# Kernel optimization log

Measured on AMD Instinct MI355X. Metric: run time of the kernel, lower is better.

The kernel has to match this reference:

```python
import jax, jax.numpy as jnp
import numpy as np

H = 12     # attention heads
W1S = 256  # one-sided sliding window (attention_window = 512)
NW = 8     # n_windows -> global tokens at each window start


def ln(x, g, b, eps=1e-5):
    m = jnp.mean(x, -1, keepdims=True)
    v = jnp.mean(jnp.square(x - m), -1, keepdims=True)
    return (x - m) * jax.lax.rsqrt(v + eps) * g + b


def _forward(x, x_mask, word_emb, pos_emb, emb_g, emb_b, Wq, bq, Wk, bk, Wv, bv, Wo, bo,
             Wqg, bqg, Wkg, bkg, Wvg, bvg, ln1_g, ln1_b, W1, b1, W2, b2, ln2_g, ln2_b,
             out_w, out_b):
    B, S = x.shape
    D = word_emb.shape[1]
    Dh = D // H
    w = W1S
    nb = S // w
    win_len = S // NW
    g = NW
    gpos = jnp.arange(g) * win_len
    scale = 1.0 / np.sqrt(Dh)

    x_mask = x_mask.at[:, gpos].set(1)  # module forces global slots to be valid
    kmask = x_mask > 0
    is_glob = jnp.zeros((S,), bool).at[gpos].set(True)

    h = ln(word_emb[x] + pos_emb[None], emb_g, emb_b)

    # static masks for the banded (sliding-window) scores
    kidx = jnp.arange(nb)[:, None] * w + jnp.arange(3 * w)[None, :] - w  # [nb,3w] abs key idx
    in_rng = (kidx >= 0) & (kidx < S)
    kidx_c = jnp.clip(kidx, 0, S - 1)
    key_ok = in_rng[None] & kmask[:, kidx_c] & (~is_glob[kidx_c])[None]   # [B,nb,3w]
    diff = jnp.arange(3 * w)[None, :] - w - jnp.arange(w)[:, None]        # [w,3w] key-query offset
    band_mask = ((jnp.abs(diff) <= w)[None, None] & key_ok[:, :, None, :]).reshape(B, 1, S, 3 * w)
    gkey_mask = kmask[:, gpos][:, None, None, :]                           # [B,1,1,g]
    mask_all = jnp.concatenate([jnp.broadcast_to(gkey_mask, (B, 1, S, g)),
                                jnp.broadcast_to(band_mask, (B, 1, S, 3 * w))], -1)

    def heads(t):
        return t.reshape(B, S, H, Dh).transpose(0, 2, 1, 3)

    def chunk3(t):  # [B,H,S,Dh] -> [B,H,nb,3w,Dh]; block n covers key offsets [-w, 2w)
        tp = jnp.pad(t, ((0, 0), (0, 0), (w, w), (0, 0))).reshape(B, H, nb + 2, w, Dh)
        return jnp.concatenate([tp[:, :, :nb], tp[:, :, 1:nb + 1], tp[:, :, 2:]], axis=3)

    def layer(h, p):
        (wq, bq_, wk, bk_, wv, bv_, wo, bo_, wqg, bqg_, wkg, bkg_, wvg, bvg_,
         g1, gb1, w1, fb1, w2, fb2, g2, gb2) = p
        q = heads(h @ wq + bq_); k = heads(h @ wk + bk_); v = heads(h @ wv + bv_)
        # sliding-window band scores + extra global-key columns, joint softmax
        sb = jnp.einsum('bhnqd,bhnkd->bhnqk', q.reshape(B, H, nb, w, Dh), chunk3(k)) * scale
        sg = jnp.einsum('bhsd,bhgd->bhsg', q, k[:, :, gpos]) * scale
        scores = jnp.concatenate([sg, sb.reshape(B, H, S, 3 * w)], -1)
        neg = jnp.finfo(scores.dtype).min * 0.5
        probs = jax.nn.softmax(jnp.where(mask_all, scores, neg), -1)
        ctx = (jnp.einsum('bhnqk,bhnkd->bhnqd', probs[..., g:].reshape(B, H, nb, w, 3 * w), chunk3(v)).reshape(B, H, S, Dh)
               + jnp.einsum('bhsg,bhgd->bhsd', probs[..., :g], v[:, :, gpos]))
        ctx = ctx.transpose(0, 2, 1, 3).reshape(B, S, D)
        # global-token queries: full attention over all keys with separate projections
        qg = (h[:, gpos] @ wqg + bqg_).reshape(B, g, H, Dh).transpose(0, 2, 1, 3)
        kg = heads(h @ wkg + bkg_); vg = heads(h @ wvg + bvg_)
        sgl = jnp.where(kmask[:, None, None, :], jnp.einsum('bhgd,bhsd->bhgs', qg, kg) * scale, neg)
        ctxg = jnp.einsum('bhgs,bhsd->bhgd', jax.nn.softmax(sgl, -1), vg).transpose(0, 2, 1, 3).reshape(B, g, D)
        ctx = ctx.at[:, gpos].set(ctxg)
        h = ln(h + ctx @ wo + bo_, g1, gb1)
        h = ln(h + jax.nn.gelu(h @ w1 + fb1, approximate=False) @ w2 + fb2, g2, gb2)
        return h, None

    params = (Wq, bq, Wk, bk, Wv, bv, Wo, bo, Wqg, bqg, Wkg, bkg, Wvg, bvg,
              ln1_g, ln1_b, W1, b1, W2, b2, ln2_g, ln2_b)
    h, _ = jax.lax.scan(jax.checkpoint(layer), h, params)
    y = h.reshape(B * NW, win_len, D)[:, 0]   # CLS pooling per window
    return y @ out_w + out_b


def setup_inputs():
    key = jax.random.key(0)
    V, S, D, L, F, O, B = 50265, 4096, 768, 12, 3072, 128, 1
    ks = iter(jax.random.split(key, 40))
    def nrm(shape):
        return (jax.random.normal(next(ks), shape) * 0.02).astype(jnp.float32)
    inp = {
        'x': jax.random.randint(next(ks), (B, S), 0, V, dtype=jnp.int32),
        'x_mask': jnp.ones((B, S), jnp.int32),
        'word_emb': nrm((V, D)), 'pos_emb': nrm((S, D)),
        'emb_g': jnp.ones((D,)), 'emb_b': jnp.zeros((D,)),
        'Wq': nrm((L, D, D)), 'bq': jnp.zeros((L, D)),
        'Wk': nrm((L, D, D)), 'bk': jnp.zeros((L, D)),
        'Wv': nrm((L, D, D)), 'bv': jnp.zeros((L, D)),
        'Wo': nrm((L, D, D)), 'bo': jnp.zeros((L, D)),
        'Wqg': nrm((L, D, D)), 'bqg': jnp.zeros((L, D)),
        'Wkg': nrm((L, D, D)), 'bkg': jnp.zeros((L, D)),
        'Wvg': nrm((L, D, D)), 'bvg': jnp.zeros((L, D)),
        'ln1_g': jnp.ones((L, D)), 'ln1_b': jnp.zeros((L, D)),
        'W1': nrm((L, D, F)), 'b1': jnp.zeros((L, F)),
        'W2': nrm((L, F, D)), 'b2': jnp.zeros((L, D)),
        'ln2_g': jnp.ones((L, D)), 'ln2_b': jnp.zeros((L, D)),
        'out_w': nrm((D, O)), 'out_b': jnp.zeros((O,)),
    }
    return inp


def reference(x, x_mask, word_emb, pos_emb, emb_g, emb_b, Wq, bq, Wk, bk, Wv, bv, Wo, bo,
              Wqg, bqg, Wkg, bkg, Wvg, bvg, ln1_g, ln1_b, W1, b1, W2, b2, ln2_g, ln2_b,
              out_w, out_b):
    return _forward(x, x_mask, word_emb, pos_emb, emb_g, emb_b, Wq, bq, Wk, bk, Wv, bv,
                    Wo, bo, Wqg, bqg, Wkg, bkg, Wvg, bvg, ln1_g, ln1_b, W1, b1, W2, b2,
                    ln2_g, ln2_b, out_w, out_b)
```

## Files before the change

### kernel.cpp

```cpp
#include <hip/hip_runtime.h>
#include <cstddef>

#define S_LEN   4096
#define DMODEL  768
#define NHEAD   12
#define DHEAD   64
#define FDIM    3072
#define NLAYER  12
#define WIN     256
#define NGLOB   8
#define GSTRIDE 512

typedef short bf16x8 __attribute__((ext_vector_type(8)));
typedef float f32x4 __attribute__((ext_vector_type(4)));
typedef unsigned short u16;

__device__ __forceinline__ u16 f2bf(float f) {
  unsigned u = __builtin_bit_cast(unsigned, f);
  return (u16)((u + 0x7FFFu + ((u >> 16) & 1u)) >> 16);
}
__device__ __forceinline__ float bf2f(u16 s) {
  unsigned u = ((unsigned)s) << 16;
  return __builtin_bit_cast(float, u);
}

__device__ __forceinline__ void gload16(const void* g, void* l) {
  __builtin_amdgcn_global_load_lds(
      (const __attribute__((address_space(1))) void*)g,
      (__attribute__((address_space(3))) void*)l, 16, 0, 0);
}

__device__ __forceinline__ float wave_sum(float v) {
#pragma unroll
  for (int off = 32; off > 0; off >>= 1) v += __shfl_xor(v, off);
  return v;
}

__device__ __forceinline__ float block_sum256(float v, float* sbuf) {
  v = wave_sum(v);
  int w = threadIdx.x >> 6;
  __syncthreads();
  if ((threadIdx.x & 63) == 0) sbuf[w] = v;
  __syncthreads();
  return sbuf[0] + sbuf[1] + sbuf[2] + sbuf[3];
}

__global__ __launch_bounds__(256) void embed_ln_kernel(
    const int* __restrict__ x, const float* __restrict__ wemb,
    const float* __restrict__ pemb, const float* __restrict__ gg,
    const float* __restrict__ bb, float* __restrict__ h, u16* __restrict__ hb) {
  __shared__ float sbuf[4];
  int s = blockIdx.x, tid = threadIdx.x;
  int idx = x[s];
  float vals[3];
#pragma unroll
  for (int i = 0; i < 3; i++) {
    int d = tid + i * 256;
    vals[i] = wemb[(size_t)idx * DMODEL + d] + pemb[(size_t)s * DMODEL + d];
  }
  float mean = block_sum256(vals[0] + vals[1] + vals[2], sbuf) * (1.0f / 768.0f);
  float sq = 0.f;
#pragma unroll
  for (int i = 0; i < 3; i++) { float t = vals[i] - mean; sq += t * t; }
  float inv = rsqrtf(block_sum256(sq, sbuf) * (1.0f / 768.0f) + 1e-5f);
#pragma unroll
  for (int i = 0; i < 3; i++) {
    int d = tid + i * 256;
    float r = (vals[i] - mean) * inv * gg[d] + bb[d];
    h[(size_t)s * DMODEL + d] = r;
    hb[(size_t)s * DMODEL + d] = f2bf(r);
  }
}

__global__ __launch_bounds__(256) void add_ln_kernel(
    float* __restrict__ h, const float* __restrict__ r,
    const float* __restrict__ gg, const float* __restrict__ bb,
    u16* __restrict__ hb) {
  __shared__ float sbuf[4];
  int s = blockIdx.x, tid = threadIdx.x;
  float vals[3];
#pragma unroll
  for (int i = 0; i < 3; i++) {
    int d = tid + i * 256;
    vals[i] = h[(size_t)s * DMODEL + d] + r[(size_t)s * DMODEL + d];
  }
  float mean = block_sum256(vals[0] + vals[1] + vals[2], sbuf) * (1.0f / 768.0f);
  float sq = 0.f;
#pragma unroll
  for (int i = 0; i < 3; i++) { float t = vals[i] - mean; sq += t * t; }
  float inv = rsqrtf(block_sum256(sq, sbuf) * (1.0f / 768.0f) + 1e-5f);
#pragma unroll
  for (int i = 0; i < 3; i++) {
    int d = tid + i * 256;
    float rr = (vals[i] - mean) * inv * gg[d] + bb[d];
    h[(size_t)s * DMODEL + d] = rr;
    hb[(size_t)s * DMODEL + d] = f2bf(rr);
  }
}

#define DD_ ((size_t)DMODEL * DMODEL)
#define DF_ ((size_t)DMODEL * FDIM)
#define WSTRIDE (6 * DD_ + 2 * DF_)
__global__ __launch_bounds__(256) void convw_kernel(
    const float* __restrict__ Wq, const float* __restrict__ Wk,
    const float* __restrict__ Wv, const float* __restrict__ Wkg,
    const float* __restrict__ Wvg, const float* __restrict__ Wo,
    const float* __restrict__ W1, const float* __restrict__ W2,
    u16* __restrict__ wt) {
  int l = blockIdx.y;
  int bid = blockIdx.x;
  const float* src; u16* dst; int K, N, r;
  u16* base = wt + (size_t)l * WSTRIDE;
  if (bid < 864) {
    int m = bid / 144; r = bid % 144; K = 768; N = 768;
    switch (m) {
      case 0: src = Wq  + l * DD_; dst = base;           break;
      case 1: src = Wk  + l * DD_; dst = base + 1 * DD_; break;
      case 2: src = Wv  + l * DD_; dst = base + 2 * DD_; break;
      case 3: src = Wkg + l * DD_; dst = base + 3 * DD_; break;
      case 4: src = Wvg + l * DD_; dst = base + 4 * DD_; break;
      default: src = Wo + l * DD_; dst = base + 5 * DD_; break;
    }
  } else if (bid < 1440) {
    r = bid - 864; K = 768; N = 3072; src = W1 + l * DF_; dst = base + 6 * DD_;
  } else {
    r = bid - 1440; K = 3072; N = 768; src = W2 + l * DF_; dst = base + 6 * DD_ + DF_;
  }
  int nt = N / 64;
  int tk = (r / nt) * 64, tn = (r % nt) * 64;
  int t = threadIdx.x;
  int c = t >> 2, ko = t & 3;
#pragma unroll
  for (int p = 0; p < 2; p++) {
    int kb = (p * 4 + ko) * 8;
    const float* sp = src + (size_t)(tk + kb) * N + tn + c;
    bf16x8 val;
#pragma unroll
    for (int j = 0; j < 8; j++) val[j] = (short)f2bf(sp[(size_t)j * N]);
    *(bf16x8*)&dst[(size_t)(tn + c) * K + tk + kb] = val;
  }
}

template <int ACT, int OUTM, int TM>
__device__ __forceinline__ void mm_core(const u16* __restrict__ A, const u16* __restrict__ Wt,
                                        const float* __restrict__ bias, void* __restrict__ Cv,
                                        int M, int N, int K, int bm, int bn,
                                        u16* As, u16* Bs) {
  constexpr int MR = TM / 32;
  constexpr int AJ = TM / 32;
  int t = threadIdx.x;
  int wid = t >> 6, lane = t & 63;
  int wr = (wid >> 1) * (TM / 2), wc = (wid & 1) * 64;
  int lr = lane & 15, lg = lane >> 4;
  f32x4 acc[MR][4];
  f32x4 zf = {0.f, 0.f, 0.f, 0.f};
#pragma unroll
  for (int m = 0; m < MR; m++)
#pragma unroll
    for (int n = 0; n < 4; n++) acc[m][n] = zf;

  int srow = wid * 8 + (lane >> 3);
  int sgr = (lane & 7) ^ (lane >> 3);
  const u16* aSrc = A + (size_t)(bm + srow) * K + sgr * 8;
  const u16* bSrc = Wt + (size_t)(bn + srow) * K + sgr * 8;
  int dstOff = wid * 8 * 64;

  for (int kt = 0; kt < K; kt += 64) {
    __syncthreads();
#pragma unroll
    for (int j = 0; j < AJ; j++)
      gload16(aSrc + kt + (size_t)j * 32 * K, As + dstOff + j * 32 * 64);
#pragma unroll
    for (int j = 0; j < 4; j++)
      gload16(bSrc + kt + (size_t)j * 32 * K, Bs + dstOff + j * 32 * 64);
    __syncthreads();
#pragma unroll
    for (int ks = 0; ks < 2; ks++) {
      bf16x8 af[MR], bfr[4];
#pragma unroll
      for (int m = 0; m < MR; m++)
        af[m] = *(const bf16x8*)&As[(wr + m * 16 + lr) * 64 + (((ks * 4 + lg) ^ (lr & 7)) * 8)];
#pragma unroll
      for (int n = 0; n < 4; n++)
        bfr[n] = *(const bf16x8*)&Bs[(wc + n * 16 + lr) * 64 + (((ks * 4 + lg) ^ (lr & 7)) * 8)];
#pragma unroll
      for (int m = 0; m < MR; m++)
#pragma unroll
        for (int n = 0; n < 4; n++)
          acc[m][n] = __builtin_amdgcn_mfma_f32_16x16x32_bf16(af[m], bfr[n], acc[m][n], 0, 0, 0);
    }
  }
#pragma unroll
  for (int n = 0; n < 4; n++) {
    int col = bn + wc + n * 16 + lr;
    float bb = bias[col];
#pragma unroll
    for (int m = 0; m < MR; m++) {
#pragma unroll
      for (int r = 0; r < 4; r++) {
        int row = bm + wr + m * 16 + lg * 4 + r;
        float xv = acc[m][n][r] + bb;
        if (ACT == 1) xv = 0.5f * xv * (1.0f + erff(xv * 0.70710678118654752f));
        if (OUTM == 0) ((float*)Cv)[(size_t)row * N + col] = xv;
        else if (OUTM == 1) ((u16*)Cv)[(size_t)row * N + col] = f2bf(xv);
        else ((u16*)Cv)[(size_t)col * M + row] = f2bf(xv);
      }
    }
  }
}

template <int ACT, int OUTM, int TM>
__global__ __launch_bounds__(256) void mm_kernel(const u16* A, const u16* Wt, const float* bias,
                                                 void* Cv, int M, int N, int K) {
  __shared__ u16 As[TM * 64];
  __shared__ u16 Bs[128 * 64];
  mm_core<ACT, OUTM, TM>(A, Wt, bias, Cv, M, N, K, blockIdx.y * TM, blockIdx.x * 128, As, Bs);
}

__global__ __launch_bounds__(256) void mm5_kernel(
    const u16* A,
    const u16* W0, const u16* W1_, const u16* W2_, const u16* W3, const u16* W4,
    const float* b0, const float* b1, const float* b2, const float* b3, const float* b4,
    u16* C0, u16* C1, u16* C2, u16* C3, u16* C4, int M, int K,
    const float* __restrict__ h, const float* __restrict__ Wqg,
    const float* __restrict__ bqg, float* __restrict__ qg) {
  __shared__ u16 As[128 * 64];
  __shared__ u16 Bs[128 * 64];
  if (blockIdx.x == 30) {
    int b = blockIdx.y;
    if (b >= 24) return;
    int gi = b / 3, c0 = (b % 3) * 256;
    int tid = threadIdx.x;
    float* hs = (float*)As;
    const float* hrow = h + (size_t)gi * GSTRIDE * DMODEL;
    for (int i = tid; i < DMODEL; i += 256) hs[i] = hrow[i];
    __syncthreads();
    float a = bqg[c0 + tid];
    for (int k = 0; k < DMODEL; k++) a += hs[k] * Wqg[(size_t)k * DMODEL + c0 + tid];
    qg[gi * DMODEL + c0 + tid] = a;
    return;
  }
  int which = blockIdx.x / 6;
  int bn = (blockIdx.x % 6) * 128;
  const u16* Ws[5] = {W0, W1_, W2_, W3, W4};
  const float* bs[5] = {b0, b1, b2, b3, b4};
  u16* Cs[5] = {C0, C1, C2, C3, C4};
  if (which == 2 || which == 4)
    mm_core<0, 2, 128>(A, Ws[which], bs[which], Cs[which], M, DMODEL, K, blockIdx.y * 128, bn, As, Bs);
  else
    mm_core<0, 1, 128>(A, Ws[which], bs[which], Cs[which], M, DMODEL, K, blockIdx.y * 128, bn, As, Bs);
}

__device__ __forceinline__ void sliding_body(
    int bid, u16* Ps,
    const u16* __restrict__ qb, const u16* __restrict__ kb,
    const u16* __restrict__ vt, const int* __restrict__ xmask,
    u16* __restrict__ ctx) {
  int hh = bid >> 5;
  int q0 = (bid & 31) * 128;
  int w = threadIdx.x >> 6, lane = threadIdx.x & 63;
  int lr = lane & 15, lg = lane >> 4;
  int rowb = q0 + w * 32;
  f32x4 zf = {0.f, 0.f, 0.f, 0.f};
  u16* Pw = Ps + w * 2048;

  bf16x8 qf[2][2];
#pragma unroll
  for (int mf = 0; mf < 2; mf++) {
    const u16* qptr = qb + (size_t)(rowb + mf * 16 + lr) * DMODEL + hh * DHEAD;
    qf[mf][0] = *(const bf16x8*)(qptr + lg * 8);
    qf[mf][1] = *(const bf16x8*)(qptr + 32 + lg * 8);
  }

  float m_run[2][4], l_run[2][4];
  f32x4 ctxa[2][4];
#pragma unroll
  for (int mf = 0; mf < 2; mf++)
#pragma unroll
    for (int r = 0; r < 4; r++) {
      m_run[mf][r] = -1e30f; l_run[mf][r] = 0.f; ctxa[mf][r] = zf;
    }

  {
    int krow = (lr < NGLOB) ? lr * GSTRIDE : 0;
    const u16* kp = kb + (size_t)krow * DMODEL + hh * DHEAD + lg * 8;
    bf16x8 kf0 = *(const bf16x8*)kp;
    bf16x8 kf1 = *(const bf16x8*)(kp + 32);
#pragma unroll
    for (int mf = 0; mf < 2; mf++) {
      f32x4 sa = __builtin_amdgcn_mfma_f32_16x16x32_bf16(qf[mf][0], kf0, zf, 0, 0, 0);
      sa = __builtin_amdgcn_mfma_f32_16x16x32_bf16(qf[mf][1], kf1, sa, 0, 0, 0);
      float p0[4], tmax[4];
#pragma unroll
      for (int r = 0; r < 4; r++) {
        float s = (lr < NGLOB) ? sa[r] * 0.125f : -1e30f;
        p0[r] = s; tmax[r] = s;
      }
#pragma unroll
      for (int o = 8; o; o >>= 1)
#pragma unroll
        for (int r = 0; r < 4; r++) tmax[r] = fmaxf(tmax[r], __shfl_xor(tmax[r], o));
      float tsum[4];
#pragma unroll
      for (int r = 0; r < 4; r++) {
        m_run[mf][r] = tmax[r];
        p0[r] = __expf(p0[r] - tmax[r]);
        tsum[r] = p0[r];
      }
#pragma unroll
      for (int o = 8; o; o >>= 1)
#pragma unroll
        for (int r = 0; r < 4; r++) tsum[r] += __shfl_xor(tsum[r], o);
#pragma unroll
      for (int r = 0; r < 4; r++) l_run[mf][r] = tsum[r];
#pragma unroll
      for (int r = 0; r < 4; r++) {
        int qi = mf * 16 + lg * 4 + r;
        Pw[qi * 64 + (((lr >> 3) ^ (qi & 7)) * 8) + (lr & 7)] = f2bf(p0[r]);
        int k2 = 16 + lr;
        Pw[qi * 64 + (((k2 >> 3) ^ (qi & 7)) * 8) + (k2 & 7)] = 0;
      }
    }
    bf16x8 pf0 = *(const bf16x8*)&Pw[lr * 64 + ((lg ^ (lr & 7)) * 8)];
    bf16x8 pf1 = *(const bf16x8*)&Pw[(16 + lr) * 64 + ((lg ^ (lr & 7)) * 8)];
#pragma unroll
    for (int c2 = 0; c2 < 4; c2++) {
      bf16x8 vg8 = {0, 0, 0, 0, 0, 0, 0, 0};
      if (lg == 0) {
        const u16* vrow = vt + (size_t)(hh * DHEAD + c2 * 16 + lr) * S_LEN;
#pragma unroll
        for (int j = 0; j < 8; j++) vg8[j] = (short)vrow[(size_t)j * GSTRIDE];
      }
      ctxa[0][c2] = __builtin_amdgcn_mfma_f32_16x16x32_bf16(pf0, vg8, ctxa[0][c2], 0, 0, 0);
      ctxa[1][c2] = __builtin_amdgcn_mfma_f32_16x16x32_bf16(pf1, vg8, ctxa[1][c2], 0, 0, 0);
    }
  }

  for (int tt = 0; tt < 10; tt++) {
    int base = q0 - WIN + tt * 64;
    if (base + 63 < 0 || base >= S_LEN) continue;
    bf16x8 kf[4][2];
    int keyc[4]; bool vc[4];
#pragma unroll
    for (int c = 0; c < 4; c++) {
      int key = base + c * 16 + lr;
      int krow = key < 0 ? 0 : (key > S_LEN - 1 ? S_LEN - 1 : key);
      vc[c] = (key >= 0) && (key < S_LEN) && ((key & (GSTRIDE - 1)) != 0) && (xmask[krow] != 0);
      keyc[c] = key;
      const u16* kp = kb + (size_t)krow * DMODEL + hh * DHEAD + lg * 8;
      kf[c][0] = *(const bf16x8*)kp;
      kf[c][1] = *(const bf16x8*)(kp + 32);
    }
#pragma unroll
    for (int mf = 0; mf < 2; mf++) {
      f32x4 sa[4];
#pragma unroll
      for (int c = 0; c < 4; c++) {
        sa[c] = __builtin_amdgcn_mfma_f32_16x16x32_bf16(qf[mf][0], kf[c][0], zf, 0, 0, 0);
        sa[c] = __builtin_amdgcn_mfma_f32_16x16x32_bf16(qf[mf][1], kf[c][1], sa[c], 0, 0, 0);
      }
      float p[4][4], tmax[4] = {-1e30f, -1e30f, -1e30f, -1e30f};
#pragma unroll
      for (int c = 0; c < 4; c++)
#pragma unroll
        for (int r = 0; r < 4; r++) {
          int qrow = rowb + mf * 16 + lg * 4 + r;
          int dd = keyc[c] - qrow;
          float s = (vc[c] && dd >= -WIN && dd <= WIN) ? sa[c][r] * 0.125f : -1e30f;
          p[c][r] = s;
          tmax[r] = fmaxf(tmax[r], s);
        }
#pragma unroll
      for (int o = 8; o; o >>= 1)
#pragma unroll
        for (int r = 0; r < 4; r++) tmax[r] = fmaxf(tmax[r], __shfl_xor(tmax[r], o));
      float sc[4], tsum[4] = {0.f, 0.f, 0.f, 0.f};
#pragma unroll
      for (int r = 0; r < 4; r++) {
        float mn = fmaxf(m_run[mf][r], tmax[r]);
        sc[r] = __expf(m_run[mf][r] - mn);
        m_run[mf][r] = mn;
      }
#pragma unroll
      for (int c = 0; c < 4; c++)
#pragma unroll
        for (int r = 0; r < 4; r++) {
          p[c][r] = __expf(p[c][r] - m_run[mf][r]);
          tsum[r] += p[c][r];
        }
#pragma unroll
      for (int o = 8; o; o >>= 1)
#pragma unroll
        for (int r = 0; r < 4; r++) tsum[r] += __shfl_xor(tsum[r], o);
#pragma unroll
      for (int r = 0; r < 4; r++) l_run[mf][r] = l_run[mf][r] * sc[r] + tsum[r];
#pragma unroll
      for (int c2 = 0; c2 < 4; c2++)
#pragma unroll
        for (int r = 0; r < 4; r++) ctxa[mf][c2][r] *= sc[r];
#pragma unroll
      for (int c = 0; c < 4; c++)
#pragma unroll
        for (int r = 0; r < 4; r++) {
          int qi = mf * 16 + lg * 4 + r, k64 = c * 16 + lr;
          Pw[qi * 64 + (((k64 >> 3) ^ (qi & 7)) * 8) + (k64 & 7)] = f2bf(p[c][r]);
        }
    }
#pragma unroll
    for (int ks = 0; ks < 2; ks++) {
      bf16x8 pf0 = *(const bf16x8*)&Pw[lr * 64 + (((ks * 4 + lg) ^ (lr & 7)) * 8)];
      bf16x8 pf1 = *(const bf16x8*)&Pw[(16 + lr) * 64 + (((ks * 4 + lg) ^ (lr & 7)) * 8)];
      int kstart = base + ks * 32 + lg * 8;
      int kc = kstart < 0 ? 0 : (kstart > S_LEN - 8 ? S_LEN - 8 : kstart);
#pragma unroll
      for (int c2 = 0; c2 < 4; c2++) {
        const u16* vp = vt + (size_t)(hh * DHEAD + c2 * 16 + lr) * S_LEN + kc;
        bf16x8 vf = *(const bf16x8*)vp;
        ctxa[0][c2] = __builtin_amdgcn_mfma_f32_16x16x32_bf16(pf0, vf, ctxa[0][c2], 0, 0, 0);
        ctxa[1][c2] = __builtin_amdgcn_mfma_f32_16x16x32_bf16(pf1, vf, ctxa[1][c2], 0, 0, 0);
      }
    }
  }

#pragma unroll
  for (int mf = 0; mf < 2; mf++)
#pragma unroll
    for (int c2 = 0; c2 < 4; c2++)
#pragma unroll
      for (int r = 0; r < 4; r++) {
        int qrow = rowb + mf * 16 + lg * 4 + r;
        ctx[(size_t)qrow * DMODEL + hh * DHEAD + c2 * 16 + lr] = f2bf(ctxa[mf][c2][r] / l_run[mf][r]);
      }
}

__device__ __forceinline__ void gattn_body(
    int hh, int c, u16* Ps,
    const float* __restrict__ qg, const u16* __restrict__ kg,
    const u16* __restrict__ vgt, const int* __restrict__ xmask,
    float* __restrict__ pm, float* __restrict__ pl, float* __restrict__ pacc) {
  int w = threadIdx.x >> 6, lane = threadIdx.x & 63;
  int lr = lane & 15, lg = lane >> 4;
  int base = c * 256 + w * 64;
  f32x4 zf = {0.f, 0.f, 0.f, 0.f};

  bf16x8 qf0, qf1;
  {
    const float* qp = qg + (size_t)(lr & 7) * DMODEL + hh * DHEAD;
    bool real = lr < 8;
#pragma unroll
    for (int j = 0; j < 8; j++) {
      qf0[j] = real ? (short)f2bf(0.125f * qp[lg * 8 + j]) : (short)0;
      qf1[j] = real ? (short)f2bf(0.125f * qp[32 + lg * 8 + j]) : (short)0;
    }
  }

  f32x4 sa[4];
  bool vc[4];
#pragma unroll
  for (int st = 0; st < 4; st++) {
    int key = base + st * 16 + lr;
    vc[st] = (xmask[key] != 0) || ((key & (GSTRIDE - 1)) == 0);
    const u16* kp = kg + (size_t)key * DMODEL + hh * DHEAD + lg * 8;
    sa[st] = __builtin_amdgcn_mfma_f32_16x16x32_bf16(qf0, *(const bf16x8*)kp, zf, 0, 0, 0);
    sa[st] = __builtin_amdgcn_mfma_f32_16x16x32_bf16(qf1, *(const bf16x8*)(kp + 32), sa[st], 0, 0, 0);
  }
  float p[4][4], tmax[4] = {-1e30f, -1e30f, -1e30f, -1e30f};
#pragma unroll
  for (int st = 0; st < 4; st++)
#pragma unroll
    for (int r = 0; r < 4; r++) {
      float s = vc[st] ? sa[st][r] : -1e30f;
      p[st][r] = s;
      tmax[r] = fmaxf(tmax[r], s);
    }
#pragma unroll
  for (int o = 8; o; o >>= 1)
#pragma unroll
    for (int r = 0; r < 4; r++) tmax[r] = fmaxf(tmax[r], __shfl_xor(tmax[r], o));
  float tsum[4] = {0.f, 0.f, 0.f, 0.f};
#pragma unroll
  for (int st = 0; st < 4; st++)
#pragma unroll
    for (int r = 0; r < 4; r++) {
      float pv = vc[st] ? __expf(p[st][r] - tmax[r]) : 0.f;
      p[st][r] = pv;
      tsum[r] += pv;
    }
#pragma unroll
  for (int o = 8; o; o >>= 1)
#pragma unroll
    for (int r = 0; r < 4; r++) tsum[r] += __shfl_xor(tsum[r], o);
#pragma unroll
  for (int st = 0; st < 4; st++)
#pragma unroll
    for (int r = 0; r < 4; r++) {
      int qi = lg * 4 + r, k64 = st * 16 + lr;
      Ps[w * 1024 + qi * 64 + (((k64 >> 3) ^ (qi & 7)) * 8) + (k64 & 7)] = f2bf(p[st][r]);
    }
  f32x4 ctxa[4] = {zf, zf, zf, zf};
#pragma unroll
  for (int ks = 0; ks < 2; ks++) {
    bf16x8 pf = *(const bf16x8*)&Ps[w * 1024 + lr * 64 + (((ks * 4 + lg) ^ (lr & 7)) * 8)];
    int kstart = base + ks * 32 + lg * 8;
#pragma unroll
    for (int c2 = 0; c2 < 4; c2++) {
      const u16* vp = vgt + (size_t)(hh * DHEAD + c2 * 16 + lr) * S_LEN + kstart;
      ctxa[c2] = __builtin_amdgcn_mfma_f32_16x16x32_bf16(pf, *(const bf16x8*)vp, ctxa[c2], 0, 0, 0);
    }
  }
  int pidx = (hh * 16 + c) * 4 + w;
  if (lg < 2) {
#pragma unroll
    for (int r = 0; r < 4; r++) {
      int q = lg * 4 + r;
#pragma unroll
      for (int c2 = 0; c2 < 4; c2++)
        pacc[(size_t)pidx * 512 + q * 64 + c2 * 16 + lr] = ctxa[c2][r];
      if (lr == 0) {
        pm[pidx * 8 + q] = tmax[r];
        pl[pidx * 8 + q] = tsum[r];
      }
    }
  }
}

__global__ __launch_bounds__(256) void attn_kernel(
    const u16* __restrict__ qb, const u16* __restrict__ kb,
    const u16* __restrict__ vt, const int* __restrict__ xmask,
    u16* __restrict__ ctx,
    const float* __restrict__ qg, const u16* __restrict__ kg,
    const u16* __restrict__ vgt,
    float* __restrict__ pm, float* __restrict__ pl, float* __restrict__ pacc) {
  __shared__ u16 Ps[4 * 32 * 64];
  int bid = blockIdx.x;
  if (bid < NHEAD * 32) {
    sliding_body(bid, Ps, qb, kb, vt, xmask, ctx);
  } else {
    int idx = bid - NHEAD * 32;
    gattn_body(idx >> 4, idx & 15, Ps, qg, kg, vgt, xmask, pm, pl, pacc);
  }
}

__global__ __launch_bounds__(64) void gattn_comb_kernel(
    const float* __restrict__ pm, const float* __restrict__ pl,
    const float* __restrict__ pacc, u16* __restrict__ ctx) {
  int gi = blockIdx.x / NHEAD, hh = blockIdx.x % NHEAD;
  int d = threadIdx.x;
  float M = -1e30f, L = 0.f, A = 0.f;
  for (int i = 0; i < 64; i++) {
    int pidx = hh * 64 + i;
    float m_i = pm[pidx * 8 + gi];
    float l_i = pl[pidx * 8 + gi];
    float a_i = pacc[(size_t)pidx * 512 + gi * 64 + d];
    if (m_i > M) {
      float sc = __expf(M - m_i);
      A = A * sc + a_i;
      L = L * sc + l_i;
      M = m_i;
    } else {
      float sc = __expf(m_i - M);
      A += a_i * sc;
      L += l_i * sc;
    }
  }
  ctx[(size_t)gi * GSTRIDE * DMODEL + hh * DHEAD + d] = f2bf(A / L);
}

__global__ __launch_bounds__(128) void cls_out_kernel(
    const float* __restrict__ h, const float* __restrict__ ow,
    const float* __restrict__ ob, float* __restrict__ y) {
  __shared__ float hs[DMODEL];
  int wi = blockIdx.x;
  int tid = threadIdx.x;
  for (int i = tid; i < DMODEL; i += 128) hs[i] = h[(size_t)wi * GSTRIDE * DMODEL + i];
  __syncthreads();
  float a = ob[tid];
  for (int d = 0; d < DMODEL; d++) a += hs[d] * ow[d * 128 + tid];
  y[wi * 128 + tid] = a;
}

extern "C" void kernel_launch(void* const* d_in, const int* in_sizes, int n_in,
                              void* d_out, int out_size, void* d_ws, size_t ws_size,
                              hipStream_t stream) {
  const int*   x      = (const int*)d_in[0];
  const int*   xmask  = (const int*)d_in[1];
  const float* wemb   = (const float*)d_in[2];
  const float* pemb   = (const float*)d_in[3];
  const float* emb_g  = (const float*)d_in[4];
  const float* emb_b  = (const float*)d_in[5];
  const float* Wq     = (const float*)d_in[6];
  const float* bq     = (const float*)d_in[7];
  const float* Wk     = (const float*)d_in[8];
  const float* bk     = (const float*)d_in[9];
  const float* Wv     = (const float*)d_in[10];
  const float* bv     = (const float*)d_in[11];
  const float* Wo     = (const float*)d_in[12];
  const float* bo     = (const float*)d_in[13];
  const float* Wqg    = (const float*)d_in[14];
  const float* bqg    = (const float*)d_in[15];
  const float* Wkg    = (const float*)d_in[16];
  const float* bkg    = (const float*)d_in[17];
  const float* Wvg    = (const float*)d_in[18];
  const float* bvg    = (const float*)d_in[19];
  const float* ln1_g  = (const float*)d_in[20];
  const float* ln1_b  = (const float*)d_in[21];
  const float* W1     = (const float*)d_in[22];
  const float* b1     = (const float*)d_in[23];
  const float* W2     = (const float*)d_in[24];
  const float* b2     = (const float*)d_in[25];
  const float* ln2_g  = (const float*)d_in[26];
  const float* ln2_b  = (const float*)d_in[27];
  const float* out_w  = (const float*)d_in[28];
  const float* out_b  = (const float*)d_in[29];

  char* wsp = (char*)d_ws;
  float* h   = (float*)wsp;  wsp += (size_t)S_LEN * DMODEL * 4;
  float* tmp = (float*)wsp;  wsp += (size_t)S_LEN * DMODEL * 4;
  u16* hb  = (u16*)wsp;      wsp += (size_t)S_LEN * DMODEL * 2;
  u16* ctx = (u16*)wsp;      wsp += (size_t)S_LEN * DMODEL * 2;
  u16* qb  = (u16*)wsp;      wsp += (size_t)S_LEN * DMODEL * 2;
  u16* kb  = (u16*)wsp;      wsp += (size_t)S_LEN * DMODEL * 2;
  u16* vt  = (u16*)wsp;      wsp += (size_t)S_LEN * DMODEL * 2;
  u16* kgb = (u16*)wsp;      wsp += (size_t)S_LEN * DMODEL * 2;
  u16* vgt = (u16*)wsp;      wsp += (size_t)S_LEN * DMODEL * 2;
  u16* mid = (u16*)wsp;      wsp += (size_t)S_LEN * FDIM * 2;
  float* qgb = (float*)wsp;  wsp += (size_t)NGLOB * DMODEL * 4;
  float* pm = (float*)wsp;   wsp += (size_t)768 * 8 * 4;
  float* pl = (float*)wsp;   wsp += (size_t)768 * 8 * 4;
  float* pacc = (float*)wsp; wsp += (size_t)768 * 512 * 4;
  u16* wtb = (u16*)wsp;      wsp += WSTRIDE * NLAYER * 2;

  embed_ln_kernel<<<S_LEN, 256, 0, stream>>>(x, wemb, pemb, emb_g, emb_b, h, hb);
  convw_kernel<<<dim3(2016, NLAYER), 256, 0, stream>>>(Wq, Wk, Wv, Wkg, Wvg, Wo, W1, W2, wtb);

  for (int l = 0; l < NLAYER; l++) {
    const float* bql  = bq  + (size_t)l * DMODEL;
    const float* bkl  = bk  + (size_t)l * DMODEL;
    const float* bvl  = bv  + (size_t)l * DMODEL;
    const float* bol  = bo  + (size_t)l * DMODEL;
    const float* wqg  = Wqg + (size_t)l * DD_;
    const float* bqgl = bqg + (size_t)l * DMODEL;
    const float* bkgl = bkg + (size_t)l * DMODEL;
    const float* bvgl = bvg + (size_t)l * DMODEL;
    const float* b1l  = b1  + (size_t)l * FDIM;
    const float* b2l  = b2  + (size_t)l * DMODEL;
    u16* base = wtb + (size_t)l * WSTRIDE;
    u16* wqT  = base;
    u16* wkT  = base + 1 * DD_;
    u16* wvT  = base + 2 * DD_;
    u16* wkgT = base + 3 * DD_;
    u16* wvgT = base + 4 * DD_;
    u16* woT  = base + 5 * DD_;
    u16* w1T  = base + 6 * DD_;
    u16* w2T  = base + 6 * DD_ + DF_;

    mm5_kernel<<<dim3(31, 32), 256, 0, stream>>>(
        hb, wqT, wkT, wvT, wkgT, wvgT, bql, bkl, bvl, bkgl, bvgl,
        qb, kb, vt, kgb, vgt, S_LEN, DMODEL, h, wqg, bqgl, qgb);

    attn_kernel<<<NHEAD * 32 + NHEAD * 16, 256, 0, stream>>>(
        qb, kb, vt, xmask, ctx, qgb, kgb, vgt, pm, pl, pacc);
    gattn_comb_kernel<<<NGLOB * NHEAD, 64, 0, stream>>>(pm, pl, pacc, ctx);

    mm_kernel<0, 0, 64><<<dim3(6, 64), 256, 0, stream>>>(ctx, woT, bol, tmp, S_LEN, DMODEL, DMODEL);
    add_ln_kernel<<<S_LEN, 256, 0, stream>>>(h, tmp, ln1_g + (size_t)l * DMODEL,
                                             ln1_b + (size_t)l * DMODEL, hb);

    mm_kernel<1, 1, 128><<<dim3(24, 32), 256, 0, stream>>>(hb, w1T, b1l, mid, S_LEN, FDIM, DMODEL);
    mm_kernel<0, 0, 64><<<dim3(6, 64), 256, 0, stream>>>(mid, w2T, b2l, tmp, S_LEN, DMODEL, FDIM);
    add_ln_kernel<<<S_LEN, 256, 0, stream>>>(h, tmp, ln2_g + (size_t)l * DMODEL,
                                             ln2_b + (size_t)l * DMODEL, hb);
  }

  cls_out_kernel<<<NGLOB, 128, 0, stream>>>(h, out_w, out_b, (float*)d_out);
}
```

Measured before the change: 3.130 ms.

## Fuse global attention combine, swizzle GEMM block order, store residual in bf16

Global-token attention now runs one block per head. Each block loops over all keys with an online softmax and combines its four waves' partial results in shared memory, which removes the separate combine kernel and the global partial buffers. The sliding-window attention no longer writes the global-token rows, and those blocks are scheduled after the global ones. The matmul kernels remap block indices with a stride-8 swizzle to improve cache reuse. The output-projection and FFN2 results are stored in bf16 instead of fp32, halving that traffic at some precision cost. The global-attention path now uses only 12 long serial blocks, which risks leaving the tail of the kernel poorly parallelised.

After: 2.945 ms. 5.9% less time.

```diff
diff --git a/kernel.cpp b/kernel.cpp
--- a/kernel.cpp
+++ b/kernel.cpp
@@ -73,7 +73,7 @@
 }
 
 __global__ __launch_bounds__(256) void add_ln_kernel(
-    float* __restrict__ h, const float* __restrict__ r,
+    float* __restrict__ h, const u16* __restrict__ r,
     const float* __restrict__ gg, const float* __restrict__ bb,
     u16* __restrict__ hb) {
   __shared__ float sbuf[4];
@@ -82,7 +82,7 @@
 #pragma unroll
   for (int i = 0; i < 3; i++) {
     int d = tid + i * 256;
-    vals[i] = h[(size_t)s * DMODEL + d] + r[(size_t)s * DMODEL + d];
+    vals[i] = h[(size_t)s * DMODEL + d] + bf2f(r[(size_t)s * DMODEL + d]);
   }
   float mean = block_sum256(vals[0] + vals[1] + vals[2], sbuf) * (1.0f / 768.0f);
   float sq = 0.f;
@@ -214,7 +214,11 @@
                                                  void* Cv, int M, int N, int K) {
   __shared__ u16 As[TM * 64];
   __shared__ u16 Bs[128 * 64];
-  mm_core<ACT, OUTM, TM>(A, Wt, bias, Cv, M, N, K, blockIdx.y * TM, blockIdx.x * 128, As, Bs);
+  int nwg = gridDim.x * gridDim.y;
+  int lin = blockIdx.y * gridDim.x + blockIdx.x;
+  int swz = (lin & 7) * (nwg >> 3) + (lin >> 3);
+  int bx = swz / gridDim.y, by = swz % gridDim.y;
+  mm_core<ACT, OUTM, TM>(A, Wt, bias, Cv, M, N, K, by * TM, bx * 128, As, Bs);
 }
 
 __global__ __launch_bounds__(256) void mm5_kernel(
@@ -240,15 +244,18 @@
     qg[gi * DMODEL + c0 + tid] = a;
     return;
   }
-  int which = blockIdx.x / 6;
-  int bn = (blockIdx.x % 6) * 128;
+  int lin = blockIdx.y * 30 + blockIdx.x;
+  int swz = (lin & 7) * 120 + (lin >> 3);
+  int bx = swz >> 5, by = swz & 31;
+  int which = bx / 6;
+  int bn = (bx % 6) * 128;
   const u16* Ws[5] = {W0, W1_, W2_, W3, W4};
   const float* bs[5] = {b0, b1, b2, b3, b4};
   u16* Cs[5] = {C0, C1, C2, C3, C4};
   if (which == 2 || which == 4)
-    mm_core<0, 2, 128>(A, Ws[which], bs[which], Cs[which], M, DMODEL, K, blockIdx.y * 128, bn, As, Bs);
+    mm_core<0, 2, 128>(A, Ws[which], bs[which], Cs[which], M, DMODEL, K, by * 128, bn, As, Bs);
   else
-    mm_core<0, 1, 128>(A, Ws[which], bs[which], Cs[which], M, DMODEL, K, blockIdx.y * 128, bn, As, Bs);
+    mm_core<0, 1, 128>(A, Ws[which], bs[which], Cs[which], M, DMODEL, K, by * 128, bn, As, Bs);
 }
 
 __device__ __forceinline__ void sliding_body(
@@ -429,19 +436,20 @@
 #pragma unroll
       for (int r = 0; r < 4; r++) {
         int qrow = rowb + mf * 16 + lg * 4 + r;
-        ctx[(size_t)qrow * DMODEL + hh * DHEAD + c2 * 16 + lr] = f2bf(ctxa[mf][c2][r] / l_run[mf][r]);
+        if ((qrow & (GSTRIDE - 1)) != 0)
+          ctx[(size_t)qrow * DMODEL + hh * DHEAD + c2 * 16 + lr] = f2bf(ctxa[mf][c2][r] / l_run[mf][r]);
       }
 }
 
 __device__ __forceinline__ void gattn_body(
-    int hh, int c, u16* Ps,
+    int hh, u16* Ps, float* cM, float* cL, float* cA,
     const float* __restrict__ qg, const u16* __restrict__ kg,
     const u16* __restrict__ vgt, const int* __restrict__ xmask,
-    float* __restrict__ pm, float* __restrict__ pl, float* __restrict__ pacc) {
+    u16* __restrict__ ctx) {
   int w = threadIdx.x >> 6, lane = threadIdx.x & 63;
   int lr = lane & 15, lg = lane >> 4;
-  int base = c * 256 + w * 64;
   f32x4 zf = {0.f, 0.f, 0.f, 0.f};
+  u16* Pw = Ps + w * 1024;
 
   bf16x8 qf0, qf1;
   {
@@ -454,73 +462,107 @@
     }
   }
 
-  f32x4 sa[4];
-  bool vc[4];
-#pragma unroll
-  for (int st = 0; st < 4; st++) {
-    int key = base + st * 16 + lr;
-    vc[st] = (xmask[key] != 0) || ((key & (GSTRIDE - 1)) == 0);
-    const u16* kp = kg + (size_t)key * DMODEL + hh * DHEAD + lg * 8;
-    sa[st] = __builtin_amdgcn_mfma_f32_16x16x32_bf16(qf0, *(const bf16x8*)kp, zf, 0, 0, 0);
-    sa[st] = __builtin_amdgcn_mfma_f32_16x16x32_bf16(qf1, *(const bf16x8*)(kp + 32), sa[st], 0, 0, 0);
-  }
-  float p[4][4], tmax[4] = {-1e30f, -1e30f, -1e30f, -1e30f};
-#pragma unroll
-  for (int st = 0; st < 4; st++)
+  float m_run[4] = {-1e30f, -1e30f, -1e30f, -1e30f};
+  float l_run[4] = {0.f, 0.f, 0.f, 0.f};
+  f32x4 ctxa[4] = {zf, zf, zf, zf};
+
+  for (int tt = w; tt < 64; tt += 4) {
+    int base = tt * 64;
+    f32x4 sa[4];
+    bool vc[4];
+#pragma unroll
+    for (int st = 0; st < 4; st++) {
+      int key = base + st * 16 + lr;
+      vc[st] = (xmask[key] != 0) || ((key & (GSTRIDE - 1)) == 0);
+      const u16* kp = kg + (size_t)key * DMODEL + hh * DHEAD + lg * 8;
+      sa[st] = __builtin_amdgcn_mfma_f32_16x16x32_bf16(qf0, *(const bf16x8*)kp, zf, 0, 0, 0);
+      sa[st] = __builtin_amdgcn_mfma_f32_16x16x32_bf16(qf1, *(const bf16x8*)(kp + 32), sa[st], 0, 0, 0);
+    }
+    float p[4][4], tmax[4] = {-1e30f, -1e30f, -1e30f, -1e30f};
+#pragma unroll
+    for (int st = 0; st < 4; st++)
+#pragma unroll
+      for (int r = 0; r < 4; r++) {
+        float s = vc[st] ? sa[st][r] : -1e30f;
+        p[st][r] = s;
+        tmax[r] = fmaxf(tmax[r], s);
+      }
+#pragma unroll
+    for (int o = 8; o; o >>= 1)
+#pragma unroll
+      for (int r = 0; r < 4; r++) tmax[r] = fmaxf(tmax[r], __shfl_xor(tmax[r], o));
+    float sc[4], tsum[4] = {0.f, 0.f, 0.f, 0.f};
 #pragma unroll
     for (int r = 0; r < 4; r++) {
-      float s = vc[st] ? sa[st][r] : -1e30f;
-      p[st][r] = s;
-      tmax[r] = fmaxf(tmax[r], s);
-    }
-#pragma unroll
-  for (int o = 8; o; o >>= 1)
-#pragma unroll
-    for (int r = 0; r < 4; r++) tmax[r] = fmaxf(tmax[r], __shfl_xor(tmax[r], o));
-  float tsum[4] = {0.f, 0.f, 0.f, 0.f};
-#pragma unroll
-  for (int st = 0; st < 4; st++)
-#pragma unroll
-    for (int r = 0; r < 4; r++) {
-      float pv = vc[st] ? __expf(p[st][r] - tmax[r]) : 0.f;
-      p[st][r] = pv;
-      tsum[r] += pv;
-    }
-#pragma unroll
-  for (int o = 8; o; o >>= 1)
-#pragma unroll
-    for (int r = 0; r < 4; r++) tsum[r] += __shfl_xor(tsum[r], o);
-#pragma unroll
-  for (int st = 0; st < 4; st++)
-#pragma unroll
-    for (int r = 0; r < 4; r++) {
-      int qi = lg * 4 + r, k64 = st * 16 + lr;
-      Ps[w * 1024 + qi * 64 + (((k64 >> 3) ^ (qi & 7)) * 8) + (k64 & 7)] = f2bf(p[st][r]);
-    }
-  f32x4 ctxa[4] = {zf, zf, zf, zf};
-#pragma unroll
-  for (int ks = 0; ks < 2; ks++) {
-    bf16x8 pf = *(const bf16x8*)&Ps[w * 1024 + lr * 64 + (((ks * 4 + lg) ^ (lr & 7)) * 8)];
-    int kstart = base + ks * 32 + lg * 8;
-#pragma unroll
-    for (int c2 = 0; c2 < 4; c2++) {
-      const u16* vp = vgt + (size_t)(hh * DHEAD + c2 * 16 + lr) * S_LEN + kstart;
-      ctxa[c2] = __builtin_amdgcn_mfma_f32_16x16x32_bf16(pf, *(const bf16x8*)vp, ctxa[c2], 0, 0, 0);
-    }
-  }
-  int pidx = (hh * 16 + c) * 4 + w;
+      float mn = fmaxf(m_run[r], tmax[r]);
+      sc[r] = __expf(m_run[r] - mn);
+      m_run[r] = mn;
+    }
+#pragma unroll
+    for (int st = 0; st < 4; st++)
+#pragma unroll
+      for (int r = 0; r < 4; r++) {
+        float pv = vc[st] ? __expf(p[st][r] - m_run[r]) : 0.f;
+        p[st][r] = pv;
+        tsum[r] += pv;
+      }
+#pragma unroll
+    for (int o = 8; o; o >>= 1)
+#pragma unroll
+      for (int r = 0; r < 4; r++) tsum[r] += __shfl_xor(tsum[r], o);
+#pragma unroll
+    for (int r = 0; r < 4; r++) l_run[r] = l_run[r] * sc[r] + tsum[r];
+#pragma unroll
+    for (int c2 = 0; c2 < 4; c2++)
+#pragma unroll
+      for (int r = 0; r < 4; r++) ctxa[c2][r] *= sc[r];
+#pragma unroll
+    for (int st = 0; st < 4; st++)
+#pragma unroll
+      for (int r = 0; r < 4; r++) {
+        int qi = lg * 4 + r, k64 = st * 16 + lr;
+        Pw[qi * 64 + (((k64 >> 3) ^ (qi & 7)) * 8) + (k64 & 7)] = f2bf(p[st][r]);
+      }
+#pragma unroll
+    for (int ks = 0; ks < 2; ks++) {
+      bf16x8 pf = *(const bf16x8*)&Pw[lr * 64 + (((ks * 4 + lg) ^ (lr & 7)) * 8)];
+      int kstart = base + ks * 32 + lg * 8;
+#pragma unroll
+      for (int c2 = 0; c2 < 4; c2++) {
+        const u16* vp = vgt + (size_t)(hh * DHEAD + c2 * 16 + lr) * S_LEN + kstart;
+        ctxa[c2] = __builtin_amdgcn_mfma_f32_16x16x32_bf16(pf, *(const bf16x8*)vp, ctxa[c2], 0, 0, 0);
+      }
+    }
+  }
+
   if (lg < 2) {
 #pragma unroll
     for (int r = 0; r < 4; r++) {
       int q = lg * 4 + r;
 #pragma unroll
       for (int c2 = 0; c2 < 4; c2++)
-        pacc[(size_t)pidx * 512 + q * 64 + c2 * 16 + lr] = ctxa[c2][r];
+        cA[(w * 8 + q) * 64 + c2 * 16 + lr] = ctxa[c2][r];
       if (lr == 0) {
-        pm[pidx * 8 + q] = tmax[r];
-        pl[pidx * 8 + q] = tsum[r];
-      }
-    }
+        cM[w * 8 + q] = m_run[r];
+        cL[w * 8 + q] = l_run[r];
+      }
+    }
+  }
+  __syncthreads();
+  int t = threadIdx.x;
+#pragma unroll
+  for (int half = 0; half < 2; half++) {
+    int slot = half * 256 + t;
+    int q = slot >> 6, d = slot & 63;
+    float M = fmaxf(fmaxf(cM[q], cM[8 + q]), fmaxf(cM[16 + q], cM[24 + q]));
+    float L = 0.f, A = 0.f;
+#pragma unroll
+    for (int ww = 0; ww < 4; ww++) {
+      float al = __expf(cM[ww * 8 + q] - M);
+      L += cL[ww * 8 + q] * al;
+      A += cA[(ww * 8 + q) * 64 + d] * al;
+    }
+    ctx[(size_t)q * GSTRIDE * DMODEL + hh * DHEAD + d] = f2bf(A / L);
   }
 }
 
@@ -529,41 +571,15 @@
     const u16* __restrict__ vt, const int* __restrict__ xmask,
     u16* __restrict__ ctx,
     const float* __restrict__ qg, const u16* __restrict__ kg,
-    const u16* __restrict__ vgt,
-    float* __restrict__ pm, float* __restrict__ pl, float* __restrict__ pacc) {
+    const u16* __restrict__ vgt) {
   __shared__ u16 Ps[4 * 32 * 64];
+  __shared__ float cM[32], cL[32], cA[32 * 64];
   int bid = blockIdx.x;
-  if (bid < NHEAD * 32) {
-    sliding_body(bid, Ps, qb, kb, vt, xmask, ctx);
+  if (bid < NHEAD) {
+    gattn_body(bid, Ps, cM, cL, cA, qg, kg, vgt, xmask, ctx);
   } else {
-    int idx = bid - NHEAD * 32;
-    gattn_body(idx >> 4, idx & 15, Ps, qg, kg, vgt, xmask, pm, pl, pacc);
-  }
-}
-
-__global__ __launch_bounds__(64) void gattn_comb_kernel(
-    const float* __restrict__ pm, const float* __restrict__ pl,
-    const float* __restrict__ pacc, u16* __restrict__ ctx) {
-  int gi = blockIdx.x / NHEAD, hh = blockIdx.x % NHEAD;
-  int d = threadIdx.x;
-  float M = -1e30f, L = 0.f, A = 0.f;
-  for (int i = 0; i < 64; i++) {
-    int pidx = hh * 64 + i;
-    float m_i = pm[pidx * 8 + gi];
-    float l_i = pl[pidx * 8 + gi];
-    float a_i = pacc[(size_t)pidx * 512 + gi * 64 + d];
-    if (m_i > M) {
-      float sc = __expf(M - m_i);
-      A = A * sc + a_i;
-      L = L * sc + l_i;
-      M = m_i;
-    } else {
-      float sc = __expf(m_i - M);
-      A += a_i * sc;
-      L += l_i * sc;
-    }
-  }
-  ctx[(size_t)gi * GSTRIDE * DMODEL + hh * DHEAD + d] = f2bf(A / L);
+    sliding_body(bid - NHEAD, Ps, qb, kb, vt, xmask, ctx);
+  }
 }
 
 __global__ __launch_bounds__(128) void cls_out_kernel(
@@ -615,7 +631,7 @@
 
   char* wsp = (char*)d_ws;
   float* h   = (float*)wsp;  wsp += (size_t)S_LEN * DMODEL * 4;
-  float* tmp = (float*)wsp;  wsp += (size_t)S_LEN * DMODEL * 4;
+  u16* tmpb  = (u16*)wsp;    wsp += (size_t)S_LEN * DMODEL * 2;
   u16* hb  = (u16*)wsp;      wsp += (size_t)S_LEN * DMODEL * 2;
   u16* ctx = (u16*)wsp;      wsp += (size_t)S_LEN * DMODEL * 2;
   u16* qb  = (u16*)wsp;      wsp += (size_t)S_LEN * DMODEL * 2;
@@ -625,9 +641,6 @@
   u16* vgt = (u16*)wsp;      wsp += (size_t)S_LEN * DMODEL * 2;
   u16* mid = (u16*)wsp;      wsp += (size_t)S_LEN * FDIM * 2;
   float* qgb = (float*)wsp;  wsp += (size_t)NGLOB * DMODEL * 4;
-  float* pm = (float*)wsp;   wsp += (size_t)768 * 8 * 4;
-  float* pl = (float*)wsp;   wsp += (size_t)768 * 8 * 4;
-  float* pacc = (float*)wsp; wsp += (size_t)768 * 512 * 4;
   u16* wtb = (u16*)wsp;      wsp += WSTRIDE * NLAYER * 2;
 
   embed_ln_kernel<<<S_LEN, 256, 0, stream>>>(x, wemb, pemb, emb_g, emb_b, h, hb);
@@ -658,17 +671,16 @@
         hb, wqT, wkT, wvT, wkgT, wvgT, bql, bkl, bvl, bkgl, bvgl,
         qb, kb, vt, kgb, vgt, S_LEN, DMODEL, h, wqg, bqgl, qgb);
 
-    attn_kernel<<<NHEAD * 32 + NHEAD * 16, 256, 0, stream>>>(
-        qb, kb, vt, xmask, ctx, qgb, kgb, vgt, pm, pl, pacc);
-    gattn_comb_kernel<<<NGLOB * NHEAD, 64, 0, stream>>>(pm, pl, pacc, ctx);
-
-    mm_kernel<0, 0, 64><<<dim3(6, 64), 256, 0, stream>>>(ctx, woT, bol, tmp, S_LEN, DMODEL, DMODEL);
-    add_ln_kernel<<<S_LEN, 256, 0, stream>>>(h, tmp, ln1_g + (size_t)l * DMODEL,
+    attn_kernel<<<NHEAD + NHEAD * 32, 256, 0, stream>>>(
+        qb, kb, vt, xmask, ctx, qgb, kgb, vgt);
+
+    mm_kernel<0, 1, 64><<<dim3(6, 64), 256, 0, stream>>>(ctx, woT, bol, tmpb, S_LEN, DMODEL, DMODEL);
+    add_ln_kernel<<<S_LEN, 256, 0, stream>>>(h, tmpb, ln1_g + (size_t)l * DMODEL,
                                              ln1_b + (size_t)l * DMODEL, hb);
 
     mm_kernel<1, 1, 128><<<dim3(24, 32), 256, 0, stream>>>(hb, w1T, b1l, mid, S_LEN, FDIM, DMODEL);
-    mm_kernel<0, 0, 64><<<dim3(6, 64), 256, 0, stream>>>(mid, w2T, b2l, tmp, S_LEN, DMODEL, FDIM);
-    add_ln_kernel<<<S_LEN, 256, 0, stream>>>(h, tmp, ln2_g + (size_t)l * DMODEL,
+    mm_kernel<0, 1, 64><<<dim3(6, 64), 256, 0, stream>>>(mid, w2T, b2l, tmpb, S_LEN, DMODEL, FDIM);
+    add_ln_kernel<<<S_LEN, 256, 0, stream>>>(h, tmpb, ln2_g + (size_t)l * DMODEL,
                                              ln2_b + (size_t)l * DMODEL, hb);
   }
 
```
